# Optimization experiments

Measured on AMD Instinct MI355X. Metric: run time of the kernel, lower is better.

The kernel has to match this reference:

```python
import jax, jax.numpy as jnp
import numpy as np


def _knn_indices(x, k):
    # Brute-force exact kNN via squared-euclidean distances (matches sklearn
    # NearestNeighbors fit on x, queried with x: self is included as a neighbor).
    sq = jnp.sum(x * x, axis=1)                      # [N]
    d = sq[:, None] + sq[None, :] - 2.0 * (x @ x.T)  # [N, N] squared distances
    _, idx = jax.lax.top_k(-d, k)                    # k smallest distances
    return idx                                        # [N, k] int32


def setup_inputs() -> dict:
    key = jax.random.key(0)
    k1, k2 = jax.random.split(key)
    N, D = 10000, 128
    return {
        "input": jax.random.normal(k1, (N, D), dtype=jnp.float32),
        "target": jax.random.normal(k2, (N, D), dtype=jnp.float32),
        "k": 15,
    }


def reference(input, target, k):
    N = input.shape[0]
    in_idx = _knn_indices(input, k)    # [N, k]
    tgt_idx = _knn_indices(target, k)  # [N, k]
    # Per-row set intersection size: neighbor indices within a row are unique,
    # so counting pairwise equality matches np.intersect1d(...).shape[0].
    matches = in_idx[:, :, None] == tgt_idx[:, None, :]  # [N, k, k]
    overlap = jnp.sum(matches)
    loss = 1.0 - overlap.astype(jnp.float32) / jnp.float32(N * k)
    return loss
```

## Files before the change

kernel.cpp:

```cpp
#include <hip/hip_runtime.h>
#include <hip/hip_bf16.h>
#include <stdint.h>

#define NROW 10000
#define DIM 128
#define NP 10240
#define KSEL 15
#define JC 32
#define NTILES (NP / 16)
#define TPC (NTILES / JC)

typedef __attribute__((ext_vector_type(4))) float f32x4;
typedef __attribute__((ext_vector_type(8))) short s16x8;
using bf16_t = __hip_bfloat16;

#define GLD16(gsrc, ldst)                                                          \
    __builtin_amdgcn_global_load_lds(                                              \
        (const __attribute__((address_space(1))) void*)(gsrc),                     \
        (__attribute__((address_space(3))) void*)(ldst), 16, 0, 0)

__global__ __launch_bounds__(256)
void knn_convert(const float* __restrict__ x0, const float* __restrict__ x1,
                 bf16_t* __restrict__ xp, float* __restrict__ sqh,
                 unsigned* __restrict__ counter)
{
    if (blockIdx.x == 0 && threadIdx.x == 0) *counter = 0u;
    const int rg   = blockIdx.x * 4 + (threadIdx.x >> 6);
    const int lane = threadIdx.x & 63;
    if (rg >= 2 * NP) return;
    const int m = rg >= NP ? 1 : 0;
    const int r = rg - m * NP;
    const float* src = m ? x1 : x0;

    float2 v = make_float2(0.f, 0.f);
    float  s = 0.f;
    if (r < NROW) {
        v = *(const float2*)(src + (size_t)r * DIM + lane * 2);
        s = v.x * v.x + v.y * v.y;
    }
    const uint32_t pk = (uint32_t)__bfloat16_as_ushort(__float2bfloat16(v.x))
                      | ((uint32_t)__bfloat16_as_ushort(__float2bfloat16(v.y)) << 16);
    const int e   = lane * 2;
    const int kk  = e >> 5;
    const int gg  = (e >> 3) & 3;
    const int pos = e & 7;
    const size_t off = ((((size_t)m * NTILES + (r >> 4)) * 4 + kk) * 64
                        + (size_t)(gg * 16 + (r & 15))) * 8 + pos;
    *(uint32_t*)(xp + off) = pk;
    #pragma unroll
    for (int o = 32; o; o >>= 1) s += __shfl_down(s, o);
    if (lane == 0) sqh[m * NP + r] = (r < NROW) ? fmaf(s, -0.5f, 1024.0f) : 1.0f;
}

#define PACKMAX(acc, idxb, Q)                                                     \
    do {                                                                          \
        const uint32_t k0_ = (__float_as_uint((acc)[0]) & 0xFFFFFC00u) | (idxb);  \
        const uint32_t k1_ = (__float_as_uint((acc)[1]) & 0xFFFFFC00u) | ((idxb) | 1u); \
        const uint32_t k2_ = (__float_as_uint((acc)[2]) & 0xFFFFFC00u) | ((idxb) | 2u); \
        const uint32_t k3_ = (__float_as_uint((acc)[3]) & 0xFFFFFC00u) | ((idxb) | 3u); \
        asm("v_max3_u32 %0, %1, %2, %0" : "+v"(Q) : "v"(k0_), "v"(k1_));          \
        asm("v_max3_u32 %0, %1, %2, %0" : "+v"(Q) : "v"(k2_), "v"(k3_));          \
    } while (0)

#define MFMA4(d, set, cin)                                                        \
    f32x4 d = __builtin_amdgcn_mfma_f32_16x16x32_bf16(a0, bfr##set[0], cin, 0, 0, 0); \
    d = __builtin_amdgcn_mfma_f32_16x16x32_bf16(a1, bfr##set[1], d, 0, 0, 0);     \
    d = __builtin_amdgcn_mfma_f32_16x16x32_bf16(a2, bfr##set[2], d, 0, 0, 0);     \
    d = __builtin_amdgcn_mfma_f32_16x16x32_bf16(a3, bfr##set[3], d, 0, 0, 0)

__global__ __launch_bounds__(256, 3)
void knn_topk(const bf16_t* __restrict__ xp, const float* __restrict__ sqh,
              uint32_t* __restrict__ pk2, uint16_t* __restrict__ px2)
{
    __shared__ bf16_t Abuf[4][2048];
    __shared__ float  Sbuf[512];

    const int m     = blockIdx.z;
    const int chunk = blockIdx.y;
    const int ib    = blockIdx.x * 256;
    const int wave  = threadIdx.x >> 6;
    const int lane  = threadIdx.x & 63;
    const int li    = lane & 15;
    const int g     = lane >> 4;
    const int tid   = threadIdx.x;

    const bf16_t* XP = xp + (size_t)m * NP * DIM;
    const float*  SQ = sqh + m * NP;

    const int t0 = chunk * TPC;
    const bf16_t* XC = XP + (size_t)t0 * 2048;
    const float*  SC = SQ + t0 * 16;

    const int ti0 = (ib >> 4) + wave * 4;
    s16x8 bfr0[4], bfr1[4], bfr2[4], bfr3[4];
    #pragma unroll
    for (int kk = 0; kk < 4; ++kk) {
        const size_t bo = ((size_t)kk * 64 + (size_t)(g * 16 + li)) * 8;
        bfr0[kk] = *(const s16x8*)(XP + (size_t)ti0 * 2048 + bo);
        bfr1[kk] = *(const s16x8*)(XP + (size_t)(ti0 + 1) * 2048 + bo);
        bfr2[kk] = *(const s16x8*)(XP + (size_t)(ti0 + 2) * 2048 + bo);
        bfr3[kk] = *(const s16x8*)(XP + (size_t)(ti0 + 3) * 2048 + bo);
    }

    if (wave < 2)
        GLD16(SC + (size_t)(wave * 64 + lane) * 4, &Sbuf[wave * 256]);
    GLD16(XC + (size_t)tid * 8, &Abuf[0][wave * 512]);
    GLD16(XC + 2048 + (size_t)tid * 8, &Abuf[1][wave * 512]);
    GLD16(XC + 2 * 2048 + (size_t)tid * 8, &Abuf[2][wave * 512]);

    uint32_t q0 = 0, q1 = 0, q2 = 0, q3 = 0;

    const bf16_t* pf = XC + 3 * 2048 + (size_t)tid * 8;

    for (int t = 0; t < TPC; ++t) {
        asm volatile("s_waitcnt vmcnt(2)" ::: "memory");
        __builtin_amdgcn_s_barrier();
        asm volatile("" ::: "memory");

        GLD16(pf, &Abuf[(t + 3) & 3][wave * 512]);
        pf += 2048;

        const bf16_t* ab = &Abuf[t & 3][lane * 8];
        const s16x8 a0 = *(const s16x8*)(ab);
        const s16x8 a1 = *(const s16x8*)(ab + 512);
        const s16x8 a2 = *(const s16x8*)(ab + 1024);
        const s16x8 a3 = *(const s16x8*)(ab + 1536);
        const f32x4 sv = *(const f32x4*)&Sbuf[t * 16 + g * 4];

        MFMA4(acc0, 0, sv);
        MFMA4(acc1, 1, sv);
        MFMA4(acc2, 2, sv);
        MFMA4(acc3, 3, sv);

        const uint32_t ib4 = (uint32_t)(t << 2);
        PACKMAX(acc0, ib4, q0);
        PACKMAX(acc1, ib4, q1);
        PACKMAX(acc2, ib4, q2);
        PACKMAX(acc3, ib4, q3);
    }

    const size_t base = ((size_t)((m * JC + chunk) * 4 + g)) * NP;
    #pragma unroll
    for (int s = 0; s < 4; ++s) {
        const uint32_t q = (s == 0) ? q0 : (s == 1) ? q1 : (s == 2) ? q2 : q3;
        const uint32_t id = q & 1023u;
        const int j = (t0 + (int)(id >> 2)) * 16 + g * 4 + (int)(id & 3u);
        const int i = ib + wave * 64 + s * 16 + li;
        pk2[base + i] = q;
        px2[base + i] = (uint16_t)j;
    }
}

#define INS(k, hi, lo) asm("v_med3_u32 %0, %1, %2, %0" : "+v"(lo) : "v"(k), "v"(hi))

__global__ __launch_bounds__(256, 1)
void knn_select_half(const uint32_t* __restrict__ pk2, const uint16_t* __restrict__ px2,
                     uint32_t* __restrict__ sk, uint16_t* __restrict__ sx)
{
    const int i = blockIdx.x * 256 + threadIdx.x;
    const int m = blockIdx.y;
    const int h = blockIdx.z;
    if (i >= NROW) return;

    const uint32_t* pv = pk2 + ((size_t)(m * 128 + h * 64)) * NP + i;
    const uint16_t* px = px2 + ((size_t)(m * 128 + h * 64)) * NP + i;

    uint32_t k[64]; uint16_t jx[64];
    #pragma unroll
    for (int c = 0; c < 64; ++c) {
        k[c]  = pv[(size_t)c * NP];
        jx[c] = px[(size_t)c * NP];
    }
    uint32_t q0 = 0, q1 = 0, q2 = 0, q3 = 0, q4 = 0, q5 = 0, q6 = 0, q7 = 0,
             q8 = 0, q9 = 0, q10 = 0, q11 = 0, q12 = 0, q13 = 0, q14 = 0;
    #pragma unroll
    for (int c = 0; c < 64; ++c) {
        const uint32_t kc = k[c];
        INS(kc, q13, q14); INS(kc, q12, q13); INS(kc, q11, q12); INS(kc, q10, q11);
        INS(kc, q9,  q10); INS(kc, q8,  q9);  INS(kc, q7,  q8);  INS(kc, q6,  q7);
        INS(kc, q5,  q6);  INS(kc, q4,  q5);  INS(kc, q3,  q4);  INS(kc, q2,  q3);
        INS(kc, q1,  q2);  INS(kc, q0,  q1);
        q0 = (q0 > kc) ? q0 : kc;
    }
    const uint32_t thr = q14;
    uint32_t* ok = sk + ((size_t)(m * 2 + h) * KSEL) * NROW + i;
    uint16_t* ox = sx + ((size_t)(m * 2 + h) * KSEL) * NROW + i;
    int n = 0;
    #pragma unroll
    for (int c = 0; c < 64; ++c) {
        if (k[c] >= thr && n < KSEL) {
            ok[(size_t)n * NROW] = k[c];
            ox[(size_t)n * NROW] = jx[c];
            n++;
        }
    }
}

__global__ __launch_bounds__(256, 1)
void knn_merge_count(const uint32_t* __restrict__ sk, const uint16_t* __restrict__ sx,
                     unsigned* __restrict__ counter)
{
    __shared__ uint16_t ids[256][KSEL + 3];
    __shared__ int wsum[4];
    const int tid  = blockIdx.x * 256 + threadIdx.x;
    const int m    = tid & 1;
    const int i    = tid >> 1;
    const int lane = threadIdx.x & 63;
    const int wave = threadIdx.x >> 6;

    if (i < NROW) {
        const uint32_t* pv = sk + (size_t)(m * 2 * KSEL) * NROW + i;
        const uint16_t* px = sx + (size_t)(m * 2 * KSEL) * NROW + i;
        uint32_t k[2 * KSEL]; uint16_t jx[2 * KSEL];
        #pragma unroll
        for (int c = 0; c < 2 * KSEL; ++c) {
            k[c]  = pv[(size_t)c * NROW];
            jx[c] = px[(size_t)c * NROW];
        }
        uint32_t q0 = 0, q1 = 0, q2 = 0, q3 = 0, q4 = 0, q5 = 0, q6 = 0, q7 = 0,
                 q8 = 0, q9 = 0, q10 = 0, q11 = 0, q12 = 0, q13 = 0, q14 = 0;
        #pragma unroll
        for (int c = 0; c < 2 * KSEL; ++c) {
            const uint32_t kc = k[c];
            INS(kc, q13, q14); INS(kc, q12, q13); INS(kc, q11, q12); INS(kc, q10, q11);
            INS(kc, q9,  q10); INS(kc, q8,  q9);  INS(kc, q7,  q8);  INS(kc, q6,  q7);
            INS(kc, q5,  q6);  INS(kc, q4,  q5);  INS(kc, q3,  q4);  INS(kc, q2,  q3);
            INS(kc, q1,  q2);  INS(kc, q0,  q1);
            q0 = (q0 > kc) ? q0 : kc;
        }
        const uint32_t thr = q14;
        int n = 0;
        #pragma unroll
        for (int c = 0; c < 2 * KSEL; ++c) {
            if (k[c] >= thr && n < KSEL) { ids[threadIdx.x][n] = jx[c]; n++; }
        }
    }
    __syncthreads();

    int cnt = 0;
    if (i < NROW && m == 0) {
        #pragma unroll
        for (int a = 0; a < KSEL; ++a) {
            const uint16_t x = ids[threadIdx.x][a];
            #pragma unroll
            for (int b = 0; b < KSEL; ++b)
                cnt += (x == ids[threadIdx.x + 1][b]) ? 1 : 0;
        }
    }
    #pragma unroll
    for (int off = 32; off; off >>= 1) cnt += __shfl_down(cnt, off);
    if (lane == 0) wsum[wave] = cnt;
    __syncthreads();
    if (threadIdx.x == 0)
        atomicAdd(counter, (unsigned)(wsum[0] + wsum[1] + wsum[2] + wsum[3]));
}

__global__ void knn_finalize(const unsigned* __restrict__ counter, float* __restrict__ out)
{
    out[0] = 1.0f - (float)(*counter) / (float)(NROW * KSEL);
}

#define XPAD (4 * 2048)
#define SQPAD 512

extern "C" void kernel_launch(void* const* d_in, const int* in_sizes, int n_in,
                              void* d_out, int out_size, void* d_ws, size_t ws_size,
                              hipStream_t stream)
{
    (void)in_sizes; (void)n_in; (void)out_size; (void)ws_size;
    const float* x0 = (const float*)d_in[0];
    const float* x1 = (const float*)d_in[1];
    float* out = (float*)d_out;

    char* ws = (char*)d_ws;
    size_t off = 0;
    bf16_t* xp  = (bf16_t*)(ws + off); off += ((size_t)2 * NP * DIM + XPAD) * sizeof(bf16_t);
    float*  sqh = (float*)(ws + off);  off += ((size_t)2 * NP + SQPAD) * sizeof(float);
    off = (off + 255) & ~(size_t)255;
    uint32_t* pk2 = (uint32_t*)(ws + off); off += (size_t)2 * JC * 4 * NP * sizeof(uint32_t);
    uint16_t* px2 = (uint16_t*)(ws + off); off += (size_t)2 * JC * 4 * NP * sizeof(uint16_t);
    off = (off + 255) & ~(size_t)255;
    uint32_t* sk = (uint32_t*)(ws + off); off += (size_t)4 * KSEL * NROW * sizeof(uint32_t);
    uint16_t* sx = (uint16_t*)(ws + off); off += (size_t)4 * KSEL * NROW * sizeof(uint16_t);
    off = (off + 255) & ~(size_t)255;
    unsigned* counter = (unsigned*)(ws + off);

    knn_convert<<<(2 * NP) / 4, 256, 0, stream>>>(x0, x1, xp, sqh, counter);
    knn_topk<<<dim3(NP / 256, JC, 2), 256, 0, stream>>>(xp, sqh, pk2, px2);
    knn_select_half<<<dim3((NROW + 255) / 256, 2, 2), 256, 0, stream>>>(pk2, px2, sk, sx);
    knn_merge_count<<<(2 * NROW + 255) / 256, 256, 0, stream>>>(sk, sx, counter);
    knn_finalize<<<1, 1, 0, stream>>>(counter, out);
}
```

Before: 75.86 us.

## Software-pipeline LDS fragment loads one tile ahead in knn_topk loop

Restructures the main MFMA loop so that the A fragments and sq values for the next tile are read from LDS right after the barrier at the end of the current iteration, with ping-pong register sets and a 2x manual unroll. The global-to-LDS prefetch is issued after the MFMAs rather than before. The aim is to hide LDS read latency behind the MFMA and pack-max work. In exchange it uses more registers under a 3-blocks-per-SM bound, and the Sbuf and its padding are doubled so all waves load it, which over-reads past the chunk's sq values.

```diff
diff --git a/kernel.cpp b/kernel.cpp
--- a/kernel.cpp
+++ b/kernel.cpp
@@ -62,18 +62,42 @@
         asm("v_max3_u32 %0, %1, %2, %0" : "+v"(Q) : "v"(k2_), "v"(k3_));          \
     } while (0)
 
-#define MFMA4(d, set, cin)                                                        \
-    f32x4 d = __builtin_amdgcn_mfma_f32_16x16x32_bf16(a0, bfr##set[0], cin, 0, 0, 0); \
-    d = __builtin_amdgcn_mfma_f32_16x16x32_bf16(a1, bfr##set[1], d, 0, 0, 0);     \
-    d = __builtin_amdgcn_mfma_f32_16x16x32_bf16(a2, bfr##set[2], d, 0, 0, 0);     \
-    d = __builtin_amdgcn_mfma_f32_16x16x32_bf16(a3, bfr##set[3], d, 0, 0, 0)
+#define MFMA4S(d, A0, A1, A2, A3, set, cin)                                       \
+    f32x4 d = __builtin_amdgcn_mfma_f32_16x16x32_bf16(A0, bfr##set[0], cin, 0, 0, 0); \
+    d = __builtin_amdgcn_mfma_f32_16x16x32_bf16(A1, bfr##set[1], d, 0, 0, 0);     \
+    d = __builtin_amdgcn_mfma_f32_16x16x32_bf16(A2, bfr##set[2], d, 0, 0, 0);     \
+    d = __builtin_amdgcn_mfma_f32_16x16x32_bf16(A3, bfr##set[3], d, 0, 0, 0)
+
+#define BODY(t, C0, C1, C2, C3, svC, N0, N1, N2, N3, svN)                         \
+    do {                                                                          \
+        MFMA4S(acc0, C0, C1, C2, C3, 0, svC);                                     \
+        MFMA4S(acc1, C0, C1, C2, C3, 1, svC);                                     \
+        MFMA4S(acc2, C0, C1, C2, C3, 2, svC);                                     \
+        MFMA4S(acc3, C0, C1, C2, C3, 3, svC);                                     \
+        GLD16(pf, &Abuf[((t) + 3) & 3][wave * 512]);                              \
+        pf += 2048;                                                               \
+        const uint32_t ib4_ = (uint32_t)((t) << 2);                               \
+        PACKMAX(acc0, ib4_, q0);                                                  \
+        PACKMAX(acc1, ib4_, q1);                                                  \
+        PACKMAX(acc2, ib4_, q2);                                                  \
+        PACKMAX(acc3, ib4_, q3);                                                  \
+        asm volatile("s_waitcnt vmcnt(2)" ::: "memory");                          \
+        __builtin_amdgcn_s_barrier();                                             \
+        asm volatile("" ::: "memory");                                            \
+        const bf16_t* nb_ = &Abuf[((t) + 1) & 3][lane * 8];                       \
+        N0 = *(const s16x8*)(nb_);                                                \
+        N1 = *(const s16x8*)(nb_ + 512);                                          \
+        N2 = *(const s16x8*)(nb_ + 1024);                                         \
+        N3 = *(const s16x8*)(nb_ + 1536);                                         \
+        svN = *(const f32x4*)&Sbuf[((t) + 1) * 16 + g * 4];                       \
+    } while (0)
 
 __global__ __launch_bounds__(256, 3)
 void knn_topk(const bf16_t* __restrict__ xp, const float* __restrict__ sqh,
               uint32_t* __restrict__ pk2, uint16_t* __restrict__ px2)
 {
     __shared__ bf16_t Abuf[4][2048];
-    __shared__ float  Sbuf[512];
+    __shared__ float  Sbuf[1024];
 
     const int m     = blockIdx.z;
     const int chunk = blockIdx.y;
@@ -102,8 +126,7 @@
         bfr3[kk] = *(const s16x8*)(XP + (size_t)(ti0 + 3) * 2048 + bo);
     }
 
-    if (wave < 2)
-        GLD16(SC + (size_t)(wave * 64 + lane) * 4, &Sbuf[wave * 256]);
+    GLD16(SC + (size_t)tid * 4, &Sbuf[wave * 256]);
     GLD16(XC + (size_t)tid * 8, &Abuf[0][wave * 512]);
     GLD16(XC + 2048 + (size_t)tid * 8, &Abuf[1][wave * 512]);
     GLD16(XC + 2 * 2048 + (size_t)tid * 8, &Abuf[2][wave * 512]);
@@ -112,31 +135,25 @@
 
     const bf16_t* pf = XC + 3 * 2048 + (size_t)tid * 8;
 
-    for (int t = 0; t < TPC; ++t) {
-        asm volatile("s_waitcnt vmcnt(2)" ::: "memory");
-        __builtin_amdgcn_s_barrier();
-        asm volatile("" ::: "memory");
-
-        GLD16(pf, &Abuf[(t + 3) & 3][wave * 512]);
-        pf += 2048;
-
-        const bf16_t* ab = &Abuf[t & 3][lane * 8];
-        const s16x8 a0 = *(const s16x8*)(ab);
-        const s16x8 a1 = *(const s16x8*)(ab + 512);
-        const s16x8 a2 = *(const s16x8*)(ab + 1024);
-        const s16x8 a3 = *(const s16x8*)(ab + 1536);
-        const f32x4 sv = *(const f32x4*)&Sbuf[t * 16 + g * 4];
-
-        MFMA4(acc0, 0, sv);
-        MFMA4(acc1, 1, sv);
-        MFMA4(acc2, 2, sv);
-        MFMA4(acc3, 3, sv);
-
-        const uint32_t ib4 = (uint32_t)(t << 2);
-        PACKMAX(acc0, ib4, q0);
-        PACKMAX(acc1, ib4, q1);
-        PACKMAX(acc2, ib4, q2);
-        PACKMAX(acc3, ib4, q3);
+    asm volatile("s_waitcnt vmcnt(2)" ::: "memory");
+    __builtin_amdgcn_s_barrier();
+    asm volatile("" ::: "memory");
+
+    s16x8 aA0, aA1, aA2, aA3, aB0, aB1, aB2, aB3;
+    f32x4 svA, svB;
+    {
+        const bf16_t* ab = &Abuf[0][lane * 8];
+        aA0 = *(const s16x8*)(ab);
+        aA1 = *(const s16x8*)(ab + 512);
+        aA2 = *(const s16x8*)(ab + 1024);
+        aA3 = *(const s16x8*)(ab + 1536);
+        svA = *(const f32x4*)&Sbuf[g * 4];
+    }
+
+    for (int p = 0; p < TPC / 2; ++p) {
+        const int t = 2 * p;
+        BODY(t,     aA0, aA1, aA2, aA3, svA, aB0, aB1, aB2, aB3, svB);
+        BODY(t + 1, aB0, aB1, aB2, aB3, svB, aA0, aA1, aA2, aA3, svA);
     }
 
     const size_t base = ((size_t)((m * JC + chunk) * 4 + g)) * NP;
@@ -261,7 +278,7 @@
 }
 
 #define XPAD (4 * 2048)
-#define SQPAD 512
+#define SQPAD 1024
 
 extern "C" void kernel_launch(void* const* d_in, const int* in_sizes, int n_in,
                               void* d_out, int out_size, void* d_ws, size_t ws_size,
```

New measurement: 73.78 us. -2.7%, faster.
